# Optimization experiments

Measured on AMD Instinct MI355X. Metric: run time of the kernel, lower is better.

The kernel has to match this reference:

```python
import jax, jax.numpy as jnp
import numpy as np

N = 100000
E = 3200000
IN_DIM = 256
HID = 128
OUT_DIM = 64


def setup_inputs() -> dict:
    key = jax.random.key(0)
    ks = jax.random.split(key, 8)
    features = jax.random.normal(ks[0], (N, IN_DIM), dtype=jnp.float32)
    edge_row = jax.random.randint(ks[1], (E,), 0, N, dtype=jnp.int32)
    edge_col = jax.random.randint(ks[2], (E,), 0, N, dtype=jnp.int32)
    edge_val = jax.random.uniform(ks[3], (E,), dtype=jnp.float32)
    W1 = jax.random.normal(ks[4], (IN_DIM, HID), dtype=jnp.float32) * (1.0 / np.sqrt(IN_DIM))
    b1 = jnp.zeros((HID,), dtype=jnp.float32)
    W2 = jax.random.normal(ks[5], (HID, OUT_DIM), dtype=jnp.float32) * (1.0 / np.sqrt(HID))
    b2 = jnp.zeros((OUT_DIM,), dtype=jnp.float32)
    return {"features": features, "edge_row": edge_row, "edge_col": edge_col,
            "edge_val": edge_val, "W1": W1, "b1": b1, "W2": W2, "b2": b2}


def reference(features, edge_row, edge_col, edge_val, W1, b1, W2, b2):
    # fc1: [N, IN_DIM] @ [IN_DIM, HID] + b1
    h = features @ W1 + b1                                   # [N, HID]
    # spmm(A, h): for each edge (r, c, v): out[r] += v * h[c]
    msgs = edge_val[:, None] * h[edge_col]                    # [E, HID] gather
    h = jax.ops.segment_sum(msgs, edge_row, num_segments=N)   # [N, HID] scatter-add
    h = jax.nn.relu(h)
    h = h @ W2 + b2                                           # [N, OUT_DIM]
    return jax.nn.log_softmax(h, axis=1)
```

## Files before the change

kernel.cpp:

```cpp
#include <hip/hip_runtime.h>
#include <math.h>

constexpr int IN_DIM  = 256;
constexpr int HID     = 128;
constexpr int OUT_DIM = 64;

constexpr int BROWS   = 128;
constexpr int NBUCK   = 782;
constexpr int CAP     = 4608;
constexpr int CAP2    = 5504;
constexpr int CHUNK   = 8192;
constexpr int GC_STRIDE = 16;

typedef short  bf16x8 __attribute__((ext_vector_type(8)));
typedef float  f32x4  __attribute__((ext_vector_type(4)));
typedef int    i32x4  __attribute__((ext_vector_type(4)));

__device__ __forceinline__ unsigned short f2bf(float x) {
    union { float f; unsigned u; } v; v.f = x;
    unsigned r = v.u + 0x7FFF + ((v.u >> 16) & 1);
    return (unsigned short)(r >> 16);
}

__global__ __launch_bounds__(256) void w1t_kernel(const float* __restrict__ W1,
                                                  unsigned short* __restrict__ W1T)
{
    int idx = blockIdx.x * 256 + threadIdx.x;
    int k = idx >> 7;
    int n = idx & 127;
    W1T[n * IN_DIM + k] = f2bf(W1[idx]);
}

__global__ __launch_bounds__(256) void w2t_kernel(const float* __restrict__ W2,
                                                  unsigned short* __restrict__ W2T)
{
    int idx = blockIdx.x * 256 + threadIdx.x;
    int k = idx >> 6;
    int n = idx & 63;
    W2T[n * HID + k] = f2bf(W2[idx]);
}

constexpr int PADK = 264;

__global__ __launch_bounds__(256) void fc1_mfma(const float* __restrict__ feat,
                                                const unsigned short* __restrict__ W1T,
                                                const float* __restrict__ b1,
                                                unsigned short* __restrict__ h1b, int N)
{
    __shared__ unsigned short sA[64 * PADK];
    const int t    = threadIdx.x;
    const int lane = t & 63;
    const int w    = t >> 6;
    const int quad = lane >> 4;
    const int ln15 = lane & 15;
    const int row0 = blockIdx.x * 64;

#pragma unroll
    for (int i = 0; i < 16; ++i) {
        int flat = i * 256 + t;
        int r    = flat >> 6;
        int k4   = flat & 63;
        int gr   = row0 + r;
        float4 v = make_float4(0.f, 0.f, 0.f, 0.f);
        if (gr < N)
            v = *(const float4*)&feat[(size_t)gr * IN_DIM + k4 * 4];
        ushort4 o;
        o.x = f2bf(v.x); o.y = f2bf(v.y); o.z = f2bf(v.z); o.w = f2bf(v.w);
        *(ushort4*)&sA[r * PADK + k4 * 4] = o;
    }
    __syncthreads();

    f32x4 acc[8];
#pragma unroll
    for (int i = 0; i < 8; ++i) acc[i] = (f32x4){0.f, 0.f, 0.f, 0.f};

#pragma unroll
    for (int ks = 0; ks < 8; ++ks) {
        bf16x8 afrag = *(const bf16x8*)&sA[(w * 16 + ln15) * PADK + ks * 32 + quad * 8];
#pragma unroll
        for (int nt = 0; nt < 8; ++nt) {
            bf16x8 bfrag = *(const bf16x8*)&W1T[(size_t)(nt * 16 + ln15) * IN_DIM + ks * 32 + quad * 8];
            acc[nt] = __builtin_amdgcn_mfma_f32_16x16x32_bf16(afrag, bfrag, acc[nt], 0, 0, 0);
        }
    }

#pragma unroll
    for (int nt = 0; nt < 8; ++nt) {
        int col = nt * 16 + ln15;
        float bias = b1[col];
#pragma unroll
        for (int r = 0; r < 4; ++r) {
            int grow = row0 + w * 16 + quad * 4 + r;
            if (grow < N)
                h1b[(size_t)grow * HID + col] = f2bf(acc[nt][r] + bias);
        }
    }
}

__global__ __launch_bounds__(256) void bin_kernel(const int* __restrict__ erow,
                                                  const int* __restrict__ ecol,
                                                  const float* __restrict__ eval,
                                                  int* __restrict__ gCursor,
                                                  int2* __restrict__ binned, int E)
{
    __shared__ int sCnt[NBUCK];
    __shared__ int sBase[NBUCK];
    const int t = threadIdx.x;
    const int e0 = blockIdx.x * CHUNK;
    const int eEnd = min(e0 + CHUNK, E);

    for (int i = t; i < NBUCK; i += 256) sCnt[i] = 0;
    __syncthreads();

    for (int e = e0 + t; e < eEnd; e += 256)
        atomicAdd(&sCnt[erow[e] >> 7], 1);
    __syncthreads();

    for (int i = t; i < NBUCK; i += 256) {
        int c = sCnt[i];
        sBase[i] = c ? atomicAdd(&gCursor[i * GC_STRIDE], c) : 0;
        sCnt[i] = 0;
    }
    __syncthreads();

    for (int e = e0 + t; e < eEnd; e += 256) {
        int   r = erow[e];
        int   c = ecol[e];
        float v = eval[e];
        int   b = r >> 7;
        int off = sBase[b] + atomicAdd(&sCnt[b], 1);
        if (off < CAP)
            binned[(size_t)b * CAP + off] = make_int2((c << 8) | ((r & 127) << 25),
                                                      __float_as_int(v));
    }
}

__global__ __launch_bounds__(256) void sort_bucket3(const int* __restrict__ gCursor,
                                                    const int2* __restrict__ binned,
                                                    int2* __restrict__ edges2,
                                                    int2* __restrict__ rowIdx, int N)
{
    __shared__ int sHist[BROWS];
    __shared__ int sStart[BROWS + 1];
    __shared__ int sCur[BROWS];
    const int t  = threadIdx.x;
    const int b  = blockIdx.x;
    const int nE = min(gCursor[b * GC_STRIDE], CAP);
    const size_t baseIn  = (size_t)b * CAP;
    const size_t baseOut = (size_t)b * CAP2;

    if (t < BROWS) sHist[t] = 0;
    __syncthreads();

    for (int i = t; i < nE; i += 256)
        atomicAdd(&sHist[(unsigned)binned[baseIn + i].x >> 25], 1);
    __syncthreads();

    if (t < BROWS) sStart[t + 1] = (sHist[t] + 7) & ~7;
    if (t == 0) sStart[0] = 0;
    __syncthreads();
    for (int o = 1; o < BROWS; o <<= 1) {
        int v = 0;
        if (t < BROWS) {
            v = sStart[t + 1];
            if (t >= o) v += sStart[t + 1 - o];
        }
        __syncthreads();
        if (t < BROWS) sStart[t + 1] = v;
        __syncthreads();
    }
    if (t < BROWS) sCur[t] = sStart[t];
    __syncthreads();

    for (int i = t; i < nE; i += 256) {
        int2 p = binned[baseIn + i];
        int rl = (unsigned)p.x >> 25;
        int pos = atomicAdd(&sCur[rl], 1);
        edges2[baseOut + pos] = p;
    }

    if (t < BROWS) {
        int h  = sHist[t];
        int ph = (h + 7) & ~7;
        size_t p0 = baseOut + sStart[t];
        for (int k = h; k < ph; ++k)
            edges2[p0 + k] = make_int2(0, 0);
        int rr = b * BROWS + t;
        if (rr < N)
            rowIdx[rr] = make_int2((int)p0, (int)(p0 + ph));
    }
}

__global__ __launch_bounds__(256) void spmm_kernel(const int2* __restrict__ rowIdx,
                                                   const int2* __restrict__ edges2,
                                                   const unsigned short* __restrict__ h1b,
                                                   unsigned* __restrict__ h2b, int N)
{
    const int lane  = threadIdx.x & 63;
    const int lane4 = lane * 4;
    const int r     = (blockIdx.x * blockDim.x + threadIdx.x) >> 6;
    if (r >= N) return;
    const char* h1base = (const char*)h1b;

    const int2 se = rowIdx[r];
    int j = se.x;
    const int jend = se.y;
    float ax = 0.f, ay = 0.f;

    for (; j + 16 <= jend; j += 16) {
        i32x4 q[8];
#pragma unroll
        for (int u = 0; u < 8; ++u)
            q[u] = __builtin_nontemporal_load((const i32x4*)&edges2[j + u * 2]);
        unsigned g[16];
#pragma unroll
        for (int u = 0; u < 8; ++u) {
            g[2 * u]     = *(const unsigned*)(h1base + (q[u].x & 0x01FFFFFF) + lane4);
            g[2 * u + 1] = *(const unsigned*)(h1base + (q[u].z & 0x01FFFFFF) + lane4);
        }
#pragma unroll
        for (int u = 0; u < 8; ++u) {
            float v0 = __int_as_float(q[u].y);
            float v1 = __int_as_float(q[u].w);
            ax += v0 * __uint_as_float(g[2 * u] << 16);
            ay += v0 * __uint_as_float(g[2 * u] & 0xFFFF0000u);
            ax += v1 * __uint_as_float(g[2 * u + 1] << 16);
            ay += v1 * __uint_as_float(g[2 * u + 1] & 0xFFFF0000u);
        }
    }
    if (j < jend) {
        i32x4 q[4];
#pragma unroll
        for (int u = 0; u < 4; ++u)
            q[u] = __builtin_nontemporal_load((const i32x4*)&edges2[j + u * 2]);
        unsigned g[8];
#pragma unroll
        for (int u = 0; u < 4; ++u) {
            g[2 * u]     = *(const unsigned*)(h1base + (q[u].x & 0x01FFFFFF) + lane4);
            g[2 * u + 1] = *(const unsigned*)(h1base + (q[u].z & 0x01FFFFFF) + lane4);
        }
#pragma unroll
        for (int u = 0; u < 4; ++u) {
            float v0 = __int_as_float(q[u].y);
            float v1 = __int_as_float(q[u].w);
            ax += v0 * __uint_as_float(g[2 * u] << 16);
            ay += v0 * __uint_as_float(g[2 * u] & 0xFFFF0000u);
            ax += v1 * __uint_as_float(g[2 * u + 1] << 16);
            ay += v1 * __uint_as_float(g[2 * u + 1] & 0xFFFF0000u);
        }
    }

    ax = fmaxf(ax, 0.f); ay = fmaxf(ay, 0.f);
    h2b[(size_t)r * 64 + lane] = (unsigned)f2bf(ax) | ((unsigned)f2bf(ay) << 16);
}

__global__ __launch_bounds__(256) void fc2_mfma(const unsigned short* __restrict__ h2b,
                                                const unsigned short* __restrict__ W2T,
                                                const float* __restrict__ b2,
                                                float* __restrict__ out, int N)
{
    const int t    = threadIdx.x;
    const int lane = t & 63;
    const int w    = t >> 6;
    const int quad = lane >> 4;
    const int ln15 = lane & 15;
    const int row0 = blockIdx.x * 64;

    int arow = row0 + w * 16 + ln15;
    if (arow >= N) arow = N - 1;

    f32x4 acc[4];
#pragma unroll
    for (int i = 0; i < 4; ++i) acc[i] = (f32x4){0.f, 0.f, 0.f, 0.f};

#pragma unroll
    for (int ks = 0; ks < 4; ++ks) {
        bf16x8 afrag = *(const bf16x8*)&h2b[(size_t)arow * HID + ks * 32 + quad * 8];
#pragma unroll
        for (int nt = 0; nt < 4; ++nt) {
            bf16x8 bfrag = *(const bf16x8*)&W2T[(size_t)(nt * 16 + ln15) * HID + ks * 32 + quad * 8];
            acc[nt] = __builtin_amdgcn_mfma_f32_16x16x32_bf16(afrag, bfrag, acc[nt], 0, 0, 0);
        }
    }

    float bias[4];
#pragma unroll
    for (int nt = 0; nt < 4; ++nt) bias[nt] = b2[nt * 16 + ln15];

#pragma unroll
    for (int r = 0; r < 4; ++r) {
        float v[4];
#pragma unroll
        for (int nt = 0; nt < 4; ++nt) v[nt] = acc[nt][r] + bias[nt];

        float m = fmaxf(fmaxf(v[0], v[1]), fmaxf(v[2], v[3]));
#pragma unroll
        for (int o = 1; o < 16; o <<= 1) m = fmaxf(m, __shfl_xor(m, o));
        float s = __expf(v[0] - m) + __expf(v[1] - m) +
                  __expf(v[2] - m) + __expf(v[3] - m);
#pragma unroll
        for (int o = 1; o < 16; o <<= 1) s += __shfl_xor(s, o);
        float ls = __logf(s);

        int grow = row0 + w * 16 + quad * 4 + r;
        if (grow < N) {
#pragma unroll
            for (int nt = 0; nt < 4; ++nt)
                out[(size_t)grow * OUT_DIM + nt * 16 + ln15] = v[nt] - m - ls;
        }
    }
}

extern "C" void kernel_launch(void* const* d_in, const int* in_sizes, int n_in,
                              void* d_out, int out_size, void* d_ws, size_t ws_size,
                              hipStream_t stream) {
    const float* feat = (const float*)d_in[0];
    const int*   erow = (const int*)d_in[1];
    const int*   ecol = (const int*)d_in[2];
    const float* eval = (const float*)d_in[3];
    const float* W1   = (const float*)d_in[4];
    const float* b1   = (const float*)d_in[5];
    const float* W2   = (const float*)d_in[6];
    const float* b2   = (const float*)d_in[7];
    float*       out  = (float*)d_out;

    const int N = in_sizes[0] / IN_DIM;
    const int E = in_sizes[1];

    unsigned short* h1b    = (unsigned short*)d_ws;
    unsigned short* h2b    = h1b + (size_t)N * HID;
    int2*           binned = (int2*)(h2b + (size_t)N * HID);
    int2*           edges2 = binned + (size_t)NBUCK * CAP;
    int2*           rowIdx = edges2 + (size_t)NBUCK * CAP2;
    unsigned short* W1T    = (unsigned short*)(rowIdx + N);
    unsigned short* W2T    = W1T + IN_DIM * HID;
    int*            gCursor= (int*)(W2T + HID * OUT_DIM);

    hipMemsetAsync(gCursor, 0, NBUCK * GC_STRIDE * sizeof(int), stream);

    w1t_kernel<<<(IN_DIM * HID) / 256, 256, 0, stream>>>(W1, W1T);
    w2t_kernel<<<(HID * OUT_DIM) / 256, 256, 0, stream>>>(W2, W2T);
    fc1_mfma<<<(N + 63) / 64, 256, 0, stream>>>(feat, W1T, b1, h1b, N);
    bin_kernel<<<(E + CHUNK - 1) / CHUNK, 256, 0, stream>>>(erow, ecol, eval,
                                                            gCursor, binned, E);
    sort_bucket3<<<NBUCK, 256, 0, stream>>>(gCursor, binned, edges2, rowIdx, N);

    const int nblk = (N + 3) / 4;
    spmm_kernel<<<nblk, 256, 0, stream>>>(rowIdx, edges2, h1b,
                                          (unsigned*)h2b, N);
    fc2_mfma<<<(N + 63) / 64, 256, 0, stream>>>(h2b, W2T, b2, out, N);
}
```

Before: 515.3 us.

## Merge weight-transpose kernels, widen bin blocks, pack spmm accumulators

Combines the W1 and W2 transpose/convert kernels into one launch to save a kernel launch. Raises the binning kernel block size from 256 to 1024 threads so each 8192-edge chunk has more parallelism and the LDS histogram setup is shared by more threads. Rewrites the spmm inner accumulation with a two-wide float vector so the compiler can emit packed FMA instructions. The changes are independent. The larger bin blocks add LDS atomic contention per block and may reduce occupancy.

```diff
diff --git a/kernel.cpp b/kernel.cpp
--- a/kernel.cpp
+++ b/kernel.cpp
@@ -14,6 +14,7 @@
 
 typedef short  bf16x8 __attribute__((ext_vector_type(8)));
 typedef float  f32x4  __attribute__((ext_vector_type(4)));
+typedef float  f32x2  __attribute__((ext_vector_type(2)));
 typedef int    i32x4  __attribute__((ext_vector_type(4)));
 
 __device__ __forceinline__ unsigned short f2bf(float x) {
@@ -22,22 +23,22 @@
     return (unsigned short)(r >> 16);
 }
 
-__global__ __launch_bounds__(256) void w1t_kernel(const float* __restrict__ W1,
-                                                  unsigned short* __restrict__ W1T)
+__global__ __launch_bounds__(256) void wt_kernel(const float* __restrict__ W1,
+                                                 const float* __restrict__ W2,
+                                                 unsigned short* __restrict__ W1T,
+                                                 unsigned short* __restrict__ W2T)
 {
     int idx = blockIdx.x * 256 + threadIdx.x;
-    int k = idx >> 7;
-    int n = idx & 127;
-    W1T[n * IN_DIM + k] = f2bf(W1[idx]);
-}
-
-__global__ __launch_bounds__(256) void w2t_kernel(const float* __restrict__ W2,
-                                                  unsigned short* __restrict__ W2T)
-{
-    int idx = blockIdx.x * 256 + threadIdx.x;
-    int k = idx >> 6;
-    int n = idx & 63;
-    W2T[n * HID + k] = f2bf(W2[idx]);
+    if (idx < IN_DIM * HID) {
+        int k = idx >> 7;
+        int n = idx & 127;
+        W1T[n * IN_DIM + k] = f2bf(W1[idx]);
+    } else {
+        int j = idx - IN_DIM * HID;
+        int k = j >> 6;
+        int n = j & 63;
+        W2T[n * HID + k] = f2bf(W2[j]);
+    }
 }
 
 constexpr int PADK = 264;
@@ -97,11 +98,11 @@
     }
 }
 
-__global__ __launch_bounds__(256) void bin_kernel(const int* __restrict__ erow,
-                                                  const int* __restrict__ ecol,
-                                                  const float* __restrict__ eval,
-                                                  int* __restrict__ gCursor,
-                                                  int2* __restrict__ binned, int E)
+__global__ __launch_bounds__(1024) void bin_kernel(const int* __restrict__ erow,
+                                                   const int* __restrict__ ecol,
+                                                   const float* __restrict__ eval,
+                                                   int* __restrict__ gCursor,
+                                                   int2* __restrict__ binned, int E)
 {
     __shared__ int sCnt[NBUCK];
     __shared__ int sBase[NBUCK];
@@ -109,21 +110,21 @@
     const int e0 = blockIdx.x * CHUNK;
     const int eEnd = min(e0 + CHUNK, E);
 
-    for (int i = t; i < NBUCK; i += 256) sCnt[i] = 0;
-    __syncthreads();
-
-    for (int e = e0 + t; e < eEnd; e += 256)
+    for (int i = t; i < NBUCK; i += 1024) sCnt[i] = 0;
+    __syncthreads();
+
+    for (int e = e0 + t; e < eEnd; e += 1024)
         atomicAdd(&sCnt[erow[e] >> 7], 1);
     __syncthreads();
 
-    for (int i = t; i < NBUCK; i += 256) {
+    for (int i = t; i < NBUCK; i += 1024) {
         int c = sCnt[i];
         sBase[i] = c ? atomicAdd(&gCursor[i * GC_STRIDE], c) : 0;
         sCnt[i] = 0;
     }
     __syncthreads();
 
-    for (int e = e0 + t; e < eEnd; e += 256) {
+    for (int e = e0 + t; e < eEnd; e += 1024) {
         int   r = erow[e];
         int   c = ecol[e];
         float v = eval[e];
@@ -205,7 +206,7 @@
     const int2 se = rowIdx[r];
     int j = se.x;
     const int jend = se.y;
-    float ax = 0.f, ay = 0.f;
+    f32x2 acc = (f32x2){0.f, 0.f};
 
     for (; j + 16 <= jend; j += 16) {
         i32x4 q[8];
@@ -220,12 +221,12 @@
         }
 #pragma unroll
         for (int u = 0; u < 8; ++u) {
-            float v0 = __int_as_float(q[u].y);
-            float v1 = __int_as_float(q[u].w);
-            ax += v0 * __uint_as_float(g[2 * u] << 16);
-            ay += v0 * __uint_as_float(g[2 * u] & 0xFFFF0000u);
-            ax += v1 * __uint_as_float(g[2 * u + 1] << 16);
-            ay += v1 * __uint_as_float(g[2 * u + 1] & 0xFFFF0000u);
+            f32x2 h0 = (f32x2){__uint_as_float(g[2 * u] << 16),
+                               __uint_as_float(g[2 * u] & 0xFFFF0000u)};
+            f32x2 h1 = (f32x2){__uint_as_float(g[2 * u + 1] << 16),
+                               __uint_as_float(g[2 * u + 1] & 0xFFFF0000u)};
+            acc += h0 * __int_as_float(q[u].y);
+            acc += h1 * __int_as_float(q[u].w);
         }
     }
     if (j < jend) {
@@ -241,16 +242,16 @@
         }
 #pragma unroll
         for (int u = 0; u < 4; ++u) {
-            float v0 = __int_as_float(q[u].y);
-            float v1 = __int_as_float(q[u].w);
-            ax += v0 * __uint_as_float(g[2 * u] << 16);
-            ay += v0 * __uint_as_float(g[2 * u] & 0xFFFF0000u);
-            ax += v1 * __uint_as_float(g[2 * u + 1] << 16);
-            ay += v1 * __uint_as_float(g[2 * u + 1] & 0xFFFF0000u);
-        }
-    }
-
-    ax = fmaxf(ax, 0.f); ay = fmaxf(ay, 0.f);
+            f32x2 h0 = (f32x2){__uint_as_float(g[2 * u] << 16),
+                               __uint_as_float(g[2 * u] & 0xFFFF0000u)};
+            f32x2 h1 = (f32x2){__uint_as_float(g[2 * u + 1] << 16),
+                               __uint_as_float(g[2 * u + 1] & 0xFFFF0000u)};
+            acc += h0 * __int_as_float(q[u].y);
+            acc += h1 * __int_as_float(q[u].w);
+        }
+    }
+
+    float ax = fmaxf(acc.x, 0.f), ay = fmaxf(acc.y, 0.f);
     h2b[(size_t)r * 64 + lane] = (unsigned)f2bf(ax) | ((unsigned)f2bf(ay) << 16);
 }
 
@@ -338,11 +339,10 @@
 
     hipMemsetAsync(gCursor, 0, NBUCK * GC_STRIDE * sizeof(int), stream);
 
-    w1t_kernel<<<(IN_DIM * HID) / 256, 256, 0, stream>>>(W1, W1T);
-    w2t_kernel<<<(HID * OUT_DIM) / 256, 256, 0, stream>>>(W2, W2T);
+    wt_kernel<<<(IN_DIM * HID + HID * OUT_DIM) / 256, 256, 0, stream>>>(W1, W2, W1T, W2T);
     fc1_mfma<<<(N + 63) / 64, 256, 0, stream>>>(feat, W1T, b1, h1b, N);
-    bin_kernel<<<(E + CHUNK - 1) / CHUNK, 256, 0, stream>>>(erow, ecol, eval,
-                                                            gCursor, binned, E);
+    bin_kernel<<<(E + CHUNK - 1) / CHUNK, 1024, 0, stream>>>(erow, ecol, eval,
+                                                             gCursor, binned, E);
     sort_bucket3<<<NBUCK, 256, 0, stream>>>(gCursor, binned, edges2, rowIdx, N);
 
     const int nblk = (N + 3) / 4;
```

Result: faster. 495.8 us (-3.8%).
